# Performance work log

Hardware: AMD Instinct MI355X
Metric: run time of the kernel (lower is better)

Reference implementation:

```python
import jax, jax.numpy as jnp
import numpy as np

EPS = 1e-5

def conv1x1(x, w, b):
    # x: [B,Cin,H,W], w: [Cout,Cin], b: [Cout]
    return jnp.einsum('oi,bihw->bohw', w, x) + b[None, :, None, None]

def self_attention(x, qw, qb, kw, kb, vw, vb, fw, fb):
    B, C, H, W = x.shape
    hid = qw.shape[0]
    q = conv1x1(x, qw, qb).reshape(B, hid, H * W).transpose(0, 2, 1)   # [B,HW,hid]
    k = conv1x1(x, kw, kb).reshape(B, hid, H * W)                      # [B,hid,HW]
    v = conv1x1(x, vw, vb).reshape(B, C, H * W)                        # [B,C,HW]
    attn = jax.nn.softmax(jnp.einsum('bnh,bhm->bnm', q, k), axis=-1)   # [B,HW,HW]
    z = jnp.einsum('bnm,bcm->bnc', attn, v)                            # [B,HW,C]
    # faithful to torch .view(B,C,H,W) on contiguous [B,HW,C]: raw reshape, no transpose
    z = z.reshape(B, C, H, W)
    return conv1x1(z * x, fw, fb) + x

def group_norm_per_channel(y, gw, gb):
    # GroupNorm(num_groups == num_channels): per-channel instance norm, biased var
    mean = y.mean(axis=(2, 3), keepdims=True)
    var = ((y - mean) ** 2).mean(axis=(2, 3), keepdims=True)
    yn = (y - mean) * jax.lax.rsqrt(var + EPS)
    return yn * gw[None, :, None, None] + gb[None, :, None, None]

def setup_inputs() -> dict:
    key = jax.random.key(0)
    ks = jax.random.split(key, 32)
    B, C, H, W = 4, 64, 64, 64
    hid, att = 64, 64
    d = {}
    d['x'] = jax.random.normal(ks[0], (B, C, H, W), jnp.float32)
    d['h'] = jax.random.normal(ks[1], (B, hid, H, W), jnp.float32)
    d['c'] = jax.random.normal(ks[2], (B, hid, H, W), jnp.float32)
    i = 3
    for pre, cin in (('ax', C), ('ah', hid)):
        for nm, cout in (('q', att), ('k', att), ('v', cin), ('f', cin)):
            d[f'{pre}_{nm}w'] = jax.random.normal(ks[i], (cout, cin), jnp.float32) * 0.05; i += 1
            d[f'{pre}_{nm}b'] = jax.random.normal(ks[i], (cout,), jnp.float32) * 0.05; i += 1
    d['conv_w'] = jax.random.normal(ks[i], (4 * hid, C + hid, 3, 3), jnp.float32) * 0.05; i += 1
    d['conv_b'] = jax.random.normal(ks[i], (4 * hid,), jnp.float32) * 0.05; i += 1
    d['gn_w'] = jnp.ones((4 * hid,), jnp.float32)
    d['gn_b'] = jnp.zeros((4 * hid,), jnp.float32)
    return d

def reference(x, h, c,
              ax_qw, ax_qb, ax_kw, ax_kb, ax_vw, ax_vb, ax_fw, ax_fb,
              ah_qw, ah_qb, ah_kw, ah_kb, ah_vw, ah_vb, ah_fw, ah_fb,
              conv_w, conv_b, gn_w, gn_b):
    hid = h.shape[1]
    xa = self_attention(x, ax_qw, ax_qb, ax_kw, ax_kb, ax_vw, ax_vb, ax_fw, ax_fb)
    ha = self_attention(h, ah_qw, ah_qb, ah_kw, ah_kb, ah_vw, ah_vb, ah_fw, ah_fb)
    combined = jnp.concatenate([xa, ha], axis=1)
    y = jax.lax.conv_general_dilated(
        combined, conv_w, window_strides=(1, 1), padding=[(1, 1), (1, 1)],
        dimension_numbers=('NCHW', 'OIHW', 'NCHW')) + conv_b[None, :, None, None]
    y = group_norm_per_channel(y, gn_w, gn_b)
    i, f, o, g = jnp.split(y, 4, axis=1)
    i = jax.nn.sigmoid(i); f = jax.nn.sigmoid(f); o = jax.nn.sigmoid(o); g = jnp.tanh(g)
    c_next = f * c + i * g
    h_next = o * jnp.tanh(c_next)
    return jnp.stack([h_next, c_next])  # [2,B,hid,H,W]
```

## Files before the change

kernel.cpp:

```cpp
#include <hip/hip_runtime.h>
#include <hip/hip_bf16.h>


typedef __hip_bfloat16 bf16;
typedef const __hip_bfloat16* bfp;
typedef short bf16x8 __attribute__((ext_vector_type(8)));
typedef short short4v __attribute__((ext_vector_type(4)));
typedef float f32x4 __attribute__((ext_vector_type(4)));
typedef float f32x16 __attribute__((ext_vector_type(16)));
typedef unsigned int u32x4 __attribute__((ext_vector_type(4)));

#define SM_SHIFT 12.0f
#define SM_A  184.66496523378733f
#define SM_B  14034.452417194552f

__device__ __forceinline__ float ldf(const void* p, long i, int f32) {
    return f32 ? ((const float*)p)[i]
               : __bfloat162float(((const bf16*)p)[i]);
}
__device__ __forceinline__ short f2bf(float f) {
    bf16 h = __float2bfloat16(f);
    return *reinterpret_cast<short*>(&h);
}
__device__ __forceinline__ float bfv(short s) {
    unsigned short u = (unsigned short)s;
    return __bfloat162float(*reinterpret_cast<const bf16*>(&u));
}

__device__ __forceinline__ int sniff_f32(const void* xr)
{
    int lane = threadIdx.x & 63;
    unsigned long long v = ((const unsigned long long*)xr)[lane];
    int ok = 0;
#pragma unroll
    for (int i = 0; i < 4; ++i) {
        int e = (int)((v >> (16 * i + 7)) & 0xFF);
        ok += (e >= 100 && e <= 141);
    }
    ok += __shfl_xor(ok, 1, 64);
    ok += __shfl_xor(ok, 2, 64);
    ok += __shfl_xor(ok, 4, 64);
    ok += __shfl_xor(ok, 8, 64);
    ok += __shfl_xor(ok, 16, 64);
    ok += __shfl_xor(ok, 32, 64);
    return ok < 200;
}

__global__ __launch_bounds__(256) void qkv_kernel(
    const void* __restrict__ Xx, const void* __restrict__ Xh,
    const void* __restrict__ qwx, const void* __restrict__ qbx,
    const void* __restrict__ kwx, const void* __restrict__ kbx,
    const void* __restrict__ vwx, const void* __restrict__ vbx,
    const void* __restrict__ qwh, const void* __restrict__ qbh,
    const void* __restrict__ kwh, const void* __restrict__ kbh,
    const void* __restrict__ vwh, const void* __restrict__ vbh,
    bf16* __restrict__ Qx, bf16* __restrict__ Kx, bf16* __restrict__ Vtx,
    bf16* __restrict__ Qh, bf16* __restrict__ Kh, bf16* __restrict__ Vth,
    const void* __restrict__ cw, bf16* __restrict__ Wt,
    float* __restrict__ gacc, int qkvN)
{
    int bx = blockIdx.x;
    int tid = threadIdx.x;
    int f32 = sniff_f32(Xx);
    if (bx >= qkvN) {
        if (bx == qkvN) {
            for (int j = 0; j < 8; ++j)
                gacc[tid * 8 + j] = 0.f;
        }
        int wi = (bx - qkvN) * 256 + tid;
        int tap = wi >> 15;
        int rem = wi & 32767;
        int oc = rem >> 7, ic = rem & 127;
        Wt[wi] = __float2bfloat16(ldf(cw, ((long)oc * 128 + ic) * 9 + tap, f32));
        return;
    }
    __shared__ __align__(16) short xt[64][72];
    __shared__ __align__(16) short wq[64][72];
    __shared__ __align__(16) short wk[64][72];
    __shared__ __align__(16) short wv[64][72];
    int ab  = (bx >> 8) & 1;
    int idx = bx & 255;
    int b = idx >> 6;
    int n0 = (idx & 63) * 64;
    int wave = tid >> 6, lane = tid & 63;
    int q = lane >> 4, l15 = lane & 15;

    const void* X = ab ? Xh : Xx;
    const void* qw = ab ? qwh : qwx; const void* qb = ab ? qbh : qbx;
    const void* kw = ab ? kwh : kwx; const void* kb = ab ? kbh : kbx;
    const void* vw = ab ? vwh : vwx; const void* vb = ab ? vbh : vbx;
    short* Qg  = (short*)(ab ? Qh  : Qx)  + (long)b * 262144;
    short* Kg  = (short*)(ab ? Kh  : Kx)  + (long)b * 262144;
    short* Vtg = (short*)(ab ? Vth : Vtx) + (long)b * 262144;

    if (!f32) {
        const short* q16 = (const short*)qw;
        const short* k16 = (const short*)kw;
        const short* v16 = (const short*)vw;
        for (int rep = 0; rep < 2; ++rep) {
            int j8 = (rep * 256 + tid) * 8;
            *(bf16x8*)&wq[j8 >> 6][j8 & 63] = *(const bf16x8*)(q16 + j8);
            *(bf16x8*)&wk[j8 >> 6][j8 & 63] = *(const bf16x8*)(k16 + j8);
            *(bf16x8*)&wv[j8 >> 6][j8 & 63] = *(const bf16x8*)(v16 + j8);
        }
    } else {
        for (int rep = 0; rep < 16; ++rep) {
            int j = rep * 256 + tid;
            int i = j >> 6, cc = j & 63;
            wq[i][cc] = f2bf(((const float*)qw)[j]);
            wk[i][cc] = f2bf(((const float*)kw)[j]);
            wv[i][cc] = f2bf(((const float*)vw)[j]);
        }
    }
    long xbase = (long)b * 262144;
    if (!f32) {
        const short* X16 = (const short*)X;
        for (int rep = 0; rep < 2; ++rep) {
            int c = rep * 32 + (tid >> 3);
            int p8 = (tid & 7) * 8;
            bf16x8 v = *(const bf16x8*)(X16 + xbase + (long)c * 4096 + n0 + p8);
#pragma unroll
            for (int j = 0; j < 8; ++j) xt[p8 + j][c] = v[j];
        }
    } else {
        for (int rep = 0; rep < 16; ++rep) {
            int c = rep * 4 + (tid >> 6);
            int p = tid & 63;
            xt[p][c] = f2bf(ldf(X, xbase + (long)c * 4096 + n0 + p, f32));
        }
    }
    __syncthreads();

    bf16x8 a0 = *(const bf16x8*)&xt[wave * 16 + l15][q * 8];
    bf16x8 a1 = *(const bf16x8*)&xt[wave * 16 + l15][32 + q * 8];

    for (int ct = 0; ct < 4; ++ct) {
        bf16x8 bq0 = *(const bf16x8*)&wq[ct * 16 + l15][q * 8];
        bf16x8 bq1 = *(const bf16x8*)&wq[ct * 16 + l15][32 + q * 8];
        f32x4 z = (f32x4){0.f, 0.f, 0.f, 0.f};
        z = __builtin_amdgcn_mfma_f32_16x16x32_bf16(a0, bq0, z, 0, 0, 0);
        z = __builtin_amdgcn_mfma_f32_16x16x32_bf16(a1, bq1, z, 0, 0, 0);
        float bias = ldf(qb, ct * 16 + l15, f32);
        for (int reg = 0; reg < 4; ++reg)
            Qg[(long)(n0 + wave * 16 + q * 4 + reg) * 64 + ct * 16 + l15] =
                f2bf(z[reg] + bias);
    }
    for (int ct = 0; ct < 4; ++ct) {
        bf16x8 bk0 = *(const bf16x8*)&wk[ct * 16 + l15][q * 8];
        bf16x8 bk1 = *(const bf16x8*)&wk[ct * 16 + l15][32 + q * 8];
        f32x4 z = (f32x4){0.f, 0.f, 0.f, 0.f};
        z = __builtin_amdgcn_mfma_f32_16x16x32_bf16(a0, bk0, z, 0, 0, 0);
        z = __builtin_amdgcn_mfma_f32_16x16x32_bf16(a1, bk1, z, 0, 0, 0);
        float bias = ldf(kb, ct * 16 + l15, f32);
        for (int reg = 0; reg < 4; ++reg)
            Kg[(long)(n0 + wave * 16 + q * 4 + reg) * 64 + ct * 16 + l15] =
                f2bf(z[reg] + bias);
    }
    bf16x8 av0 = *(const bf16x8*)&wv[wave * 16 + l15][q * 8];
    bf16x8 av1 = *(const bf16x8*)&wv[wave * 16 + l15][32 + q * 8];
    for (int ct = 0; ct < 4; ++ct) {
        bf16x8 bx0 = *(const bf16x8*)&xt[ct * 16 + l15][q * 8];
        bf16x8 bx1 = *(const bf16x8*)&xt[ct * 16 + l15][32 + q * 8];
        f32x4 z = (f32x4){0.f, 0.f, 0.f, 0.f};
        z = __builtin_amdgcn_mfma_f32_16x16x32_bf16(av0, bx0, z, 0, 0, 0);
        z = __builtin_amdgcn_mfma_f32_16x16x32_bf16(av1, bx1, z, 0, 0, 0);
        for (int reg = 0; reg < 4; ++reg) {
            int c_out = wave * 16 + q * 4 + reg;
            float bias = ldf(vb, c_out, f32);
            Vtg[(long)c_out * 4096 + n0 + ct * 16 + l15] = f2bf(z[reg] + bias);
        }
    }
}

__global__ __launch_bounds__(256, 2) void attn_kernel(
    bfp Qx, bfp Kx, bfp Vtx,
    const void* __restrict__ Xx, const void* __restrict__ fwx,
    const void* __restrict__ fbx, bf16* __restrict__ outx,
    bfp Qh, bfp Kh, bfp Vth,
    const void* __restrict__ Xh, const void* __restrict__ fwh,
    const void* __restrict__ fbh, bf16* __restrict__ outh)
{
    __shared__ __align__(16) short smem[16384];
    short (*ks)[64][64]  = (short (*)[64][64])(smem);
    short (*vts)[64][64] = (short (*)[64][64])(smem + 8192);

    int tid = threadIdx.x;
    int wave = tid >> 6, lane = tid & 63;
    int l31 = lane & 31, hi = lane >> 5;
    int nh = wave >> 1, mh = wave & 1;
    int ab  = blockIdx.x >> 8;
    int idx = blockIdx.x & 255;
    int b = idx >> 6;
    int hrow = idx & 63;
    int f32 = sniff_f32(Xx);

    const short* Qb  = (const short*)(ab ? Qh  : Qx)  + (long)b * 262144;
    const short* Kb  = (const short*)(ab ? Kh  : Kx)  + (long)b * 262144;
    const short* Vtb = (const short*)(ab ? Vth : Vtx) + (long)b * 262144;
    const void* X  = ab ? Xh  : Xx;
    const void* fw = ab ? fwh : fwx;
    const void* fb = ab ? fbh : fbx;
    bf16* out = ab ? outh : outx;
    long xbase = (long)b * 262144;

    int cnq = nh * 32 + l31;
    long nq = (long)cnq * 64 + hrow;
    bf16x8 aq[4];
#pragma unroll
    for (int kc = 0; kc < 4; ++kc)
        aq[kc] = *(const bf16x8*)(Qb + nq * 64 + kc * 16 + hi * 8);

    f32x16 acc0 = (f32x16)(0.0f);
    f32x16 acc1 = (f32x16)(0.0f);
    f32x16 acc_l = (f32x16)(0.0f);
    const short ONE = 0x3F80;
    const bf16x8 ones = {ONE, ONE, ONE, ONE, ONE, ONE, ONE, ONE};

    int sw = (l31 >> 1) & 7;

    int r0 = tid >> 3, r1 = r0 + 32;
    int g = tid & 7;
    int sr0 = (r0 & 51) | ((r0 & 4) << 1) | ((r0 & 8) >> 1);
    int sr1 = sr0 + 32;
    int gk = (g ^ ((sr0 >> 1) & 7)) << 3;
    int gv = (g ^ ((r0 >> 1) & 7)) << 3;

    bf16x8 pk0 = *(const bf16x8*)(Kb + (long)r0 * 64 + g * 8);
    bf16x8 pk1 = *(const bf16x8*)(Kb + (long)r1 * 64 + g * 8);
    bf16x8 pv0 = *(const bf16x8*)(Vtb + (long)r0 * 4096 + g * 8);
    bf16x8 pv1 = *(const bf16x8*)(Vtb + (long)r1 * 4096 + g * 8);

    for (int it = 0; it < 64; ++it) {
        int buf = it & 1;
        *(bf16x8*)&ks[buf][sr0][gk] = pk0;
        *(bf16x8*)&ks[buf][sr1][gk] = pk1;
        *(bf16x8*)&vts[buf][r0][gv] = pv0;
        *(bf16x8*)&vts[buf][r1][gv] = pv1;
        __syncthreads();
        if (it + 1 < 64) {
            long m = (long)(it + 1) * 64;
            pk0 = *(const bf16x8*)(Kb + (m + r0) * 64 + g * 8);
            pk1 = *(const bf16x8*)(Kb + (m + r1) * 64 + g * 8);
            pv0 = *(const bf16x8*)(Vtb + (long)r0 * 4096 + m + g * 8);
            pv1 = *(const bf16x8*)(Vtb + (long)r1 * 4096 + m + g * 8);
        }

        f32x16 s = (f32x16)(0.0f);
        const short* kbase = &ks[buf][mh * 32 + l31][0];
#pragma unroll
        for (int kc = 0; kc < 4; ++kc) {
            bf16x8 ak = *(const bf16x8*)(kbase + (((kc * 2 + hi) ^ sw) << 3));
            s = __builtin_amdgcn_mfma_f32_32x32x16_bf16(ak, aq[kc], s, 0, 0, 0);
        }

        unsigned P32[8];
#pragma unroll
        for (int i = 0; i < 8; ++i) {
            unsigned b0 = (unsigned)fmaxf(fmaf(s[2 * i],     SM_A, SM_B), 0.f);
            unsigned b1 = (unsigned)fmaxf(fmaf(s[2 * i + 1], SM_A, SM_B), 0.f);
            P32[i] = b0 | (b1 << 16);
        }
        u32x4 B0v = (u32x4){P32[0], P32[1], P32[2], P32[3]};
        u32x4 B1v = (u32x4){P32[4], P32[5], P32[6], P32[7]};
        bf16x8 bp0 = __builtin_bit_cast(bf16x8, B0v);
        bf16x8 bp1 = __builtin_bit_cast(bf16x8, B1v);

        acc_l = __builtin_amdgcn_mfma_f32_32x32x16_bf16(ones, bp0, acc_l, 0, 0, 0);
        acc_l = __builtin_amdgcn_mfma_f32_32x32x16_bf16(ones, bp1, acc_l, 0, 0, 0);

        const short* v0base = &vts[buf][l31][0];
        const short* v1base = &vts[buf][32 + l31][0];
#pragma unroll
        for (int mc = 0; mc < 2; ++mc) {
            int gm = ((mh * 4 + mc * 2 + hi) ^ sw) << 3;
            bf16x8 av0 = *(const bf16x8*)(v0base + gm);
            bf16x8 av1 = *(const bf16x8*)(v1base + gm);
            bf16x8 bp = mc ? bp1 : bp0;
            acc0 = __builtin_amdgcn_mfma_f32_32x32x16_bf16(av0, bp, acc0, 0, 0, 0);
            acc1 = __builtin_amdgcn_mfma_f32_32x32x16_bf16(av1, bp, acc1, 0, 0, 0);
        }
    }

    float l_acc = acc_l[0];

    float* fs = (float*)smem;
    float* fl = (float*)smem + 4096;
    short* at_s  = smem;
    short* fwt_s = smem + 4992;
    short* o_lds = smem + 9600;

    __syncthreads();
    if (mh == 1) {
#pragma unroll
        for (int r = 0; r < 16; ++r) {
            int row = (r & 3) + ((r >> 2) << 3) + (hi << 2);
            fs[nh * 2048 + row * 32 + l31]        = acc0[r];
            fs[nh * 2048 + 1024 + row * 32 + l31] = acc1[r];
        }
        if (lane < 32) fl[nh * 32 + l31] = l_acc;
    }
    __syncthreads();
    if (mh == 0) {
        float iln = 1.f / (l_acc + fl[nh * 32 + l31]);
        short* orow = o_lds + cnq * 68;
#pragma unroll
        for (int rq = 0; rq < 4; ++rq) {
            int c0 = rq * 8 + (hi << 2);
            short4v oa, ob;
#pragma unroll
            for (int j = 0; j < 4; ++j) {
                int r = rq * 4 + j;
                int row = (r & 3) + ((r >> 2) << 3) + (hi << 2);
                oa[j] = f2bf((acc0[r] + fs[nh * 2048 + row * 32 + l31]) * iln);
                ob[j] = f2bf((acc1[r] + fs[nh * 2048 + 1024 + row * 32 + l31]) * iln);
            }
            *(short4v*)(orow + c0)      = oa;
            *(short4v*)(orow + 32 + c0) = ob;
        }
    }
    __syncthreads();
    if (!f32) {
        const short* f16p = (const short*)fw;
        for (int rep = 0; rep < 2; ++rep) {
            int j8 = (rep * 256 + tid) * 8;
            *(bf16x8*)(fwt_s + (j8 >> 6) * 72 + (j8 & 63)) =
                *(const bf16x8*)(f16p + j8);
        }
    } else {
        for (int rep = 0; rep < 16; ++rep) {
            int j = rep * 256 + tid;
            fwt_s[(j >> 6) * 72 + (j & 63)] = f2bf(((const float*)fw)[j]);
        }
    }
    {
        int cn = tid >> 3;
        int w8 = (tid & 7) * 8;
        for (int rep = 0; rep < 2; ++rep, cn += 32) {
            if (!f32) {
                bf16x8 xv = *(const bf16x8*)(
                    (const short*)X + xbase + (long)cn * 4096 + hrow * 64 + w8);
#pragma unroll
                for (int j = 0; j < 8; ++j)
                    at_s[(w8 + j) * 78 + cn] =
                        f2bf(bfv(o_lds[cn * 68 + w8 + j]) * bfv(xv[j]));
            } else {
#pragma unroll
                for (int j = 0; j < 8; ++j)
                    at_s[(w8 + j) * 78 + cn] =
                        f2bf(bfv(o_lds[cn * 68 + w8 + j]) *
                             ((const float*)X)[xbase + (long)cn * 4096 + hrow * 64 + w8 + j]);
            }
        }
    }
    __syncthreads();
    {
        int q = lane >> 4, l15 = lane & 15;
        bf16x8 a0 = *(const bf16x8*)(fwt_s + (wave * 16 + l15) * 72 + q * 8);
        bf16x8 a1 = *(const bf16x8*)(fwt_s + (wave * 16 + l15) * 72 + 32 + q * 8);
        short* outp = (short*)out;
        for (int nt = 0; nt < 4; ++nt) {
            bf16x8 b0 = *(const bf16x8*)(at_s + (nt * 16 + l15) * 78 + q * 8);
            bf16x8 b1 = *(const bf16x8*)(at_s + (nt * 16 + l15) * 78 + 32 + q * 8);
            f32x4 z = (f32x4){0.f, 0.f, 0.f, 0.f};
            z = __builtin_amdgcn_mfma_f32_16x16x32_bf16(a0, b0, z, 0, 0, 0);
            z = __builtin_amdgcn_mfma_f32_16x16x32_bf16(a1, b1, z, 0, 0, 0);
            int w = nt * 16 + l15;
            short4v o4;
            for (int reg = 0; reg < 4; ++reg) {
                int o = wave * 16 + q * 4 + reg;
                float v = z[reg] + ldf(fb, o, f32) +
                          ldf(X, xbase + (long)o * 4096 + hrow * 64 + w, f32);
                o4[reg] = f2bf(v);
            }
            *(short4v*)(outp + (((long)(b * 64 + hrow) * 64 + w) * 64
                                + wave * 16 + q * 4)) = o4;
        }
    }
}

__global__ __launch_bounds__(256) void conv3x3_kernel(
    bfp xa, bfp ha, bfp Wt, const void* __restrict__ cb,
    bf16* __restrict__ y, float* __restrict__ gacc,
    const void* __restrict__ xraw)
{
    __shared__ __align__(16) short in_s[3][66][136];
    int f32 = sniff_f32(xraw);
    int bx = blockIdx.x;
    int b = bx >> 7;
    int rem = bx & 127;
    int h = rem >> 1;
    int halfoc = rem & 1;
    int tid = threadIdx.x;
    int wave = tid >> 6, lane = tid & 63;
    int q = lane >> 4, l15 = lane & 15;

    const short* xab = (const short*)xa + (long)b * 262144;
    const short* hab = (const short*)ha + (long)b * 262144;
    const bf16x8 zv = {0, 0, 0, 0, 0, 0, 0, 0};
    for (int r = 0; r < 3; ++r) {
        int gy = h + r - 1;
        bool valid = (gy >= 0) && (gy < 64);
        for (int s = 0; s < 2; ++s) {
            int strip = s * 256 + tid;
            int w = strip >> 3;
            int c8 = (strip & 7) * 8;
            bf16x8 vx = zv, vh = zv;
            if (valid) {
                vx = *(const bf16x8*)(xab + ((long)gy * 64 + w) * 64 + c8);
                vh = *(const bf16x8*)(hab + ((long)gy * 64 + w) * 64 + c8);
            }
            *(bf16x8*)&in_s[r][w + 1][c8]      = vx;
            *(bf16x8*)&in_s[r][w + 1][64 + c8] = vh;
        }
    }
    if (tid < 96) {
        int r = tid / 32;
        int rest = tid % 32;
        int col = (rest & 1) ? 65 : 0;
        int c8 = (rest >> 1) * 8;
        *(bf16x8*)&in_s[r][col][c8] = zv;
    }
    __syncthreads();

    int oc0 = halfoc * 128 + wave * 32;
    f32x4 acc[2][4];
    for (int mt = 0; mt < 2; ++mt)
        for (int nt = 0; nt < 4; ++nt)
            acc[mt][nt] = (f32x4){0.f, 0.f, 0.f, 0.f};

    const short* Wb = (const short*)Wt;
    for (int tap = 0; tap < 9; ++tap) {
        int dy = tap / 3, dx = tap - dy * 3;
        for (int kc = 0; kc < 4; ++kc) {
            bf16x8 afrag[2];
            for (int mt = 0; mt < 2; ++mt)
                afrag[mt] = *(const bf16x8*)(
                    Wb + ((long)tap * 256 + oc0 + mt * 16 + l15) * 128 + kc * 32 + q * 8);
            for (int nt = 0; nt < 4; ++nt) {
                bf16x8 bfrag = *(const bf16x8*)&in_s[dy][nt * 16 + l15 + dx][kc * 32 + q * 8];
                for (int mt = 0; mt < 2; ++mt)
                    acc[mt][nt] = __builtin_amdgcn_mfma_f32_16x16x32_bf16(
                        afrag[mt], bfrag, acc[mt][nt], 0, 0, 0);
            }
        }
    }

    long ybase = (long)b * 1048576 + (long)h * 64;
    for (int mt = 0; mt < 2; ++mt) {
        for (int reg = 0; reg < 4; ++reg) {
            int oc = oc0 + mt * 16 + q * 4 + reg;
            float bias = ldf(cb, oc, f32);
            float s = 0.f, s2 = 0.f;
            for (int nt = 0; nt < 4; ++nt) {
                float v = acc[mt][nt][reg] + bias;
                ((short*)y)[ybase + (long)oc * 4096 + nt * 16 + l15] = f2bf(v);
                s += v; s2 = fmaf(v, v, s2);
            }
            s  += __shfl_xor(s,  1, 64);  s2 += __shfl_xor(s2, 1, 64);
            s  += __shfl_xor(s,  2, 64);  s2 += __shfl_xor(s2, 2, 64);
            s  += __shfl_xor(s,  4, 64);  s2 += __shfl_xor(s2, 4, 64);
            s  += __shfl_xor(s,  8, 64);  s2 += __shfl_xor(s2, 8, 64);
            if (l15 == 0) {
                atomicAdd(&gacc[b * 256 + oc], s);
                atomicAdd(&gacc[1024 + b * 256 + oc], s2);
            }
        }
    }
}

__global__ __launch_bounds__(256) void gates_kernel(
    bfp y, const float* __restrict__ gacc,
    const void* __restrict__ gw, const void* __restrict__ gb,
    const void* __restrict__ c_in, void* __restrict__ out)
{
    int f32 = sniff_f32(c_in);
    int t = blockIdx.x * 256 + threadIdx.x;
    int b = t >> 15;
    int r = t & 32767;
    int ch = r >> 9;
    int p8 = (r & 511) * 8;
    long ybase = (long)b * 1048576;
    long idx8 = (long)b * 262144 + (long)ch * 4096 + p8;

    float mu[4], rstd[4], gwv[4], gbv[4];
    bf16x8 yv[4];
#pragma unroll
    for (int g = 0; g < 4; ++g) {
        int cc = g * 64 + ch;
        float m = gacc[b * 256 + cc] * (1.f / 4096.f);
        float var = gacc[1024 + b * 256 + cc] * (1.f / 4096.f) - m * m;
        mu[g] = m;
        rstd[g] = rsqrtf(fmaxf(var, 0.f) + 1e-5f);
        gwv[g] = ldf(gw, cc, f32);
        gbv[g] = ldf(gb, cc, f32);
        yv[g] = *(const bf16x8*)((const short*)y + ybase + (long)cc * 4096 + p8);
    }
    float cprev[8];
    if (!f32) {
        bf16x8 cv = *(const bf16x8*)((const short*)c_in + idx8);
#pragma unroll
        for (int j = 0; j < 8; ++j) cprev[j] = bfv(cv[j]);
    } else {
#pragma unroll
        for (int j = 0; j < 8; ++j) cprev[j] = ((const float*)c_in)[idx8 + j];
    }
    bf16x8 hn8, cn8;
    float hnf[8], cnf[8];
#pragma unroll
    for (int j = 0; j < 8; ++j) {
        float v0 = (bfv(yv[0][j]) - mu[0]) * rstd[0] * gwv[0] + gbv[0];
        float v1 = (bfv(yv[1][j]) - mu[1]) * rstd[1] * gwv[1] + gbv[1];
        float v2 = (bfv(yv[2][j]) - mu[2]) * rstd[2] * gwv[2] + gbv[2];
        float v3 = (bfv(yv[3][j]) - mu[3]) * rstd[3] * gwv[3] + gbv[3];
        float ig = 1.f / (1.f + __expf(-v0));
        float fg = 1.f / (1.f + __expf(-v1));
        float og = 1.f / (1.f + __expf(-v2));
        float gg = tanhf(v3);
        float cn = fg * cprev[j] + ig * gg;
        float hn = og * tanhf(cn);
        hn8[j] = f2bf(hn); cn8[j] = f2bf(cn);
        hnf[j] = hn; cnf[j] = cn;
    }
    if (f32) {
        float* o32 = (float*)out;
#pragma unroll
        for (int j = 0; j < 8; ++j) {
            o32[idx8 + j] = hnf[j];
            o32[1048576 + idx8 + j] = cnf[j];
        }
    } else {
        short* o16 = (short*)out;
        *(bf16x8*)(o16 + idx8) = hn8;
        *(bf16x8*)(o16 + 1048576 + idx8) = cn8;
    }
}

extern "C" void kernel_launch(void* const* d_in, const int* in_sizes, int n_in,
                              void* d_out, int out_size, void* d_ws, size_t ws_size,
                              hipStream_t stream)
{
    const void* x = d_in[0]; const void* h = d_in[1]; const void* c = d_in[2];
    const void* ax_qw = d_in[3],  *ax_qb = d_in[4];
    const void* ax_kw = d_in[5],  *ax_kb = d_in[6];
    const void* ax_vw = d_in[7],  *ax_vb = d_in[8];
    const void* ax_fw = d_in[9],  *ax_fb = d_in[10];
    const void* ah_qw = d_in[11], *ah_qb = d_in[12];
    const void* ah_kw = d_in[13], *ah_kb = d_in[14];
    const void* ah_vw = d_in[15], *ah_vb = d_in[16];
    const void* ah_fw = d_in[17], *ah_fb = d_in[18];
    const void* conv_w = d_in[19], *conv_b = d_in[20];
    const void* gn_w = d_in[21],  *gn_b = d_in[22];

    char* wsb = (char*)d_ws;
    auto S = [&](int i) { return wsb + ((unsigned long)i << 21); };
    bool fused = ws_size >= (18ul << 20) + 16384;

    bf16* ha = (bf16*)S(0);
    bf16* Wt = (bf16*)S(1);
    bf16 *Qx, *Kx, *Vtx, *Qh, *Kh, *Vth, *xa, *y;
    char* tail;
    if (fused) {
        Qx = (bf16*)S(2); Kx = (bf16*)S(3); Vtx = (bf16*)S(4);
        Qh = (bf16*)S(5); Kh = (bf16*)S(6); Vth = (bf16*)S(7);
        xa = (bf16*)S(8); y = Qx;
        tail = S(9);
    } else {
        Qx = (bf16*)S(2); Kx = (bf16*)S(3); Vtx = (bf16*)S(4);
        Qh = Qx; Kh = Kx; Vth = Vtx;
        xa = (bf16*)S(6); y = Qx;
        tail = S(7);
    }
    float* gacc = (float*)tail;

    if (fused) {
        qkv_kernel<<<512 + 1152, 256, 0, stream>>>(
            x, h,
            ax_qw, ax_qb, ax_kw, ax_kb, ax_vw, ax_vb,
            ah_qw, ah_qb, ah_kw, ah_kb, ah_vw, ah_vb,
            Qx, Kx, Vtx, Qh, Kh, Vth, conv_w, Wt, gacc, 512);
        attn_kernel<<<512, 256, 0, stream>>>(
            Qx, Kx, Vtx, x, ax_fw, ax_fb, xa,
            Qh, Kh, Vth, h, ah_fw, ah_fb, ha);
    } else {
        qkv_kernel<<<256 + 1152, 256, 0, stream>>>(
            x, x,
            ax_qw, ax_qb, ax_kw, ax_kb, ax_vw, ax_vb,
            ax_qw, ax_qb, ax_kw, ax_kb, ax_vw, ax_vb,
            Qx, Kx, Vtx, Qx, Kx, Vtx, conv_w, Wt, gacc, 256);
        attn_kernel<<<256, 256, 0, stream>>>(
            Qx, Kx, Vtx, x, ax_fw, ax_fb, xa,
            Qx, Kx, Vtx, x, ax_fw, ax_fb, xa);
        qkv_kernel<<<256, 256, 0, stream>>>(
            h, h,
            ah_qw, ah_qb, ah_kw, ah_kb, ah_vw, ah_vb,
            ah_qw, ah_qb, ah_kw, ah_kb, ah_vw, ah_vb,
            Qh, Kh, Vth, Qh, Kh, Vth, conv_w, Wt, gacc, 256);
        attn_kernel<<<256, 256, 0, stream>>>(
            Qh, Kh, Vth, h, ah_fw, ah_fb, ha,
            Qh, Kh, Vth, h, ah_fw, ah_fb, ha);
    }
    conv3x3_kernel<<<512, 256, 0, stream>>>(xa, ha, Wt, conv_b, y, gacc, x);
    gates_kernel<<<512, 256, 0, stream>>>(y, gacc, gn_w, gn_b, c, d_out);
}
```

Measured before the change: 202.4 us.

## Widen attention blocks to 8 waves with 128-key tiles and 4-way key split

The attention kernel moves from 256 to 512 threads per block. Each KV iteration now stages 128 keys instead of 64, so the loop runs 32 times and there are half as many barriers. Four waves per query half now split the key dimension, and their partial outputs and row sums are reduced through LDS in two stages. The output-projection epilogue is split across all 8 waves, and the fw staging is overlapped with the reduction. In exchange, LDS doubles to 64 KB per block, which may limit occupancy, and the extra reduction passes and barriers add cost.

Measured after the change: 201.6 us. About the same (-0.4%).

```diff
diff --git a/kernel.cpp b/kernel.cpp
--- a/kernel.cpp
+++ b/kernel.cpp
@@ -172,7 +172,7 @@
     }
 }
 
-__global__ __launch_bounds__(256, 2) void attn_kernel(
+__global__ __launch_bounds__(512, 4) void attn_kernel(
     bfp Qx, bfp Kx, bfp Vtx,
     const void* __restrict__ Xx, const void* __restrict__ fwx,
     const void* __restrict__ fbx, bf16* __restrict__ outx,
@@ -180,14 +180,12 @@
     const void* __restrict__ Xh, const void* __restrict__ fwh,
     const void* __restrict__ fbh, bf16* __restrict__ outh)
 {
-    __shared__ __align__(16) short smem[16384];
-    short (*ks)[64][64]  = (short (*)[64][64])(smem);
-    short (*vts)[64][64] = (short (*)[64][64])(smem + 8192);
+    __shared__ __align__(16) short smem[32768];
 
     int tid = threadIdx.x;
     int wave = tid >> 6, lane = tid & 63;
     int l31 = lane & 31, hi = lane >> 5;
-    int nh = wave >> 1, mh = wave & 1;
+    int nh = wave >> 2, mq = wave & 3;
     int ab  = blockIdx.x >> 8;
     int idx = blockIdx.x & 255;
     int b = idx >> 6;
@@ -210,43 +208,48 @@
     for (int kc = 0; kc < 4; ++kc)
         aq[kc] = *(const bf16x8*)(Qb + nq * 64 + kc * 16 + hi * 8);
 
-    f32x16 acc0 = (f32x16)(0.0f);
-    f32x16 acc1 = (f32x16)(0.0f);
+    f32x16 acc[2];
+    acc[0] = (f32x16)(0.0f); acc[1] = (f32x16)(0.0f);
     f32x16 acc_l = (f32x16)(0.0f);
     const short ONE = 0x3F80;
     const bf16x8 ones = {ONE, ONE, ONE, ONE, ONE, ONE, ONE, ONE};
 
     int sw = (l31 >> 1) & 7;
 
-    int r0 = tid >> 3, r1 = r0 + 32;
+    int r0 = tid >> 3, r1 = r0 + 64;
     int g = tid & 7;
     int sr0 = (r0 & 51) | ((r0 & 4) << 1) | ((r0 & 8) >> 1);
-    int sr1 = sr0 + 32;
+    int sr1 = sr0 + 64;
     int gk = (g ^ ((sr0 >> 1) & 7)) << 3;
-    int gv = (g ^ ((r0 >> 1) & 7)) << 3;
+    int cV = r0;
+    int gv = (g ^ (cV & 7)) << 3;
 
     bf16x8 pk0 = *(const bf16x8*)(Kb + (long)r0 * 64 + g * 8);
     bf16x8 pk1 = *(const bf16x8*)(Kb + (long)r1 * 64 + g * 8);
-    bf16x8 pv0 = *(const bf16x8*)(Vtb + (long)r0 * 4096 + g * 8);
-    bf16x8 pv1 = *(const bf16x8*)(Vtb + (long)r1 * 4096 + g * 8);
-
-    for (int it = 0; it < 64; ++it) {
-        int buf = it & 1;
-        *(bf16x8*)&ks[buf][sr0][gk] = pk0;
-        *(bf16x8*)&ks[buf][sr1][gk] = pk1;
-        *(bf16x8*)&vts[buf][r0][gv] = pv0;
-        *(bf16x8*)&vts[buf][r1][gv] = pv1;
+    bf16x8 pv0 = *(const bf16x8*)(Vtb + (long)cV * 4096 + g * 8);
+    bf16x8 pv1 = *(const bf16x8*)(Vtb + (long)cV * 4096 + 64 + g * 8);
+
+    for (int mt = 0; mt < 32; ++mt) {
+        int buf = mt & 1;
+        short* ksw = smem + buf * 8192;
+        short* vsw = smem + 16384 + buf * 8192;
+        *(bf16x8*)(ksw + sr0 * 64 + gk)      = pk0;
+        *(bf16x8*)(ksw + sr1 * 64 + gk)      = pk1;
+        *(bf16x8*)(vsw + cV * 128 + gv)      = pv0;
+        *(bf16x8*)(vsw + cV * 128 + gv + 64) = pv1;
         __syncthreads();
-        if (it + 1 < 64) {
-            long m = (long)(it + 1) * 64;
+        if (mt + 1 < 32) {
+            long m = (long)(mt + 1) * 128;
             pk0 = *(const bf16x8*)(Kb + (m + r0) * 64 + g * 8);
             pk1 = *(const bf16x8*)(Kb + (m + r1) * 64 + g * 8);
-            pv0 = *(const bf16x8*)(Vtb + (long)r0 * 4096 + m + g * 8);
-            pv1 = *(const bf16x8*)(Vtb + (long)r1 * 4096 + m + g * 8);
-        }
+            pv0 = *(const bf16x8*)(Vtb + (long)cV * 4096 + m + g * 8);
+            pv1 = *(const bf16x8*)(Vtb + (long)cV * 4096 + m + 64 + g * 8);
+        }
+        const short* ksb  = smem + buf * 8192;
+        const short* vtsb = smem + 16384 + buf * 8192;
 
         f32x16 s = (f32x16)(0.0f);
-        const short* kbase = &ks[buf][mh * 32 + l31][0];
+        const short* kbase = ksb + (mq * 32 + l31) * 64;
 #pragma unroll
         for (int kc = 0; kc < 4; ++kc) {
             bf16x8 ak = *(const bf16x8*)(kbase + (((kc * 2 + hi) ^ sw) << 3));
@@ -268,97 +271,121 @@
         acc_l = __builtin_amdgcn_mfma_f32_32x32x16_bf16(ones, bp0, acc_l, 0, 0, 0);
         acc_l = __builtin_amdgcn_mfma_f32_32x32x16_bf16(ones, bp1, acc_l, 0, 0, 0);
 
-        const short* v0base = &vts[buf][l31][0];
-        const short* v1base = &vts[buf][32 + l31][0];
 #pragma unroll
         for (int mc = 0; mc < 2; ++mc) {
-            int gm = ((mh * 4 + mc * 2 + hi) ^ sw) << 3;
-            bf16x8 av0 = *(const bf16x8*)(v0base + gm);
-            bf16x8 av1 = *(const bf16x8*)(v1base + gm);
             bf16x8 bp = mc ? bp1 : bp0;
-            acc0 = __builtin_amdgcn_mfma_f32_32x32x16_bf16(av0, bp, acc0, 0, 0, 0);
-            acc1 = __builtin_amdgcn_mfma_f32_32x32x16_bf16(av1, bp, acc1, 0, 0, 0);
+            int qch = mq * 4 + mc * 2 + hi;
+#pragma unroll
+            for (int ch = 0; ch < 2; ++ch) {
+                int c = ch * 32 + l31;
+                bf16x8 av = *(const bf16x8*)(
+                    vtsb + c * 128 + ((qch ^ (c & 7)) << 3));
+                acc[ch] = __builtin_amdgcn_mfma_f32_32x32x16_bf16(av, bp, acc[ch], 0, 0, 0);
+            }
         }
     }
 
     float l_acc = acc_l[0];
 
     float* fs = (float*)smem;
-    float* fl = (float*)smem + 4096;
+    float* fl = (float*)smem + 8192;
+    short* fwt_s = smem + 16896;
+    short* o_lds = smem + 21504;
     short* at_s  = smem;
-    short* fwt_s = smem + 4992;
-    short* o_lds = smem + 9600;
-
-    __syncthreads();
-    if (mh == 1) {
-#pragma unroll
-        for (int r = 0; r < 16; ++r) {
-            int row = (r & 3) + ((r >> 2) << 3) + (hi << 2);
-            fs[nh * 2048 + row * 32 + l31]        = acc0[r];
-            fs[nh * 2048 + 1024 + row * 32 + l31] = acc1[r];
-        }
-        if (lane < 32) fl[nh * 32 + l31] = l_acc;
-    }
-    __syncthreads();
-    if (mh == 0) {
-        float iln = 1.f / (l_acc + fl[nh * 32 + l31]);
+
+    __syncthreads();
+    if (hi == 0) fl[nh * 128 + mq * 32 + l31] = l_acc;
+    if (mq == 1 || mq == 3) {
+        int L = mq >> 1;
+#pragma unroll
+        for (int ch = 0; ch < 2; ++ch)
+#pragma unroll
+            for (int r = 0; r < 16; ++r) {
+                int c = ch * 32 + (r & 3) + ((r >> 2) << 3) + (hi << 2);
+                fs[L * 4096 + nh * 2048 + c * 32 + l31] = acc[ch][r];
+            }
+    }
+    if (!f32) {
+        int j8 = tid * 8;
+        *(bf16x8*)(fwt_s + (j8 >> 6) * 72 + (j8 & 63)) =
+            *(const bf16x8*)((const short*)fw + j8);
+    } else {
+#pragma unroll
+        for (int jj = 0; jj < 8; ++jj) {
+            int j = tid * 8 + jj;
+            fwt_s[(j >> 6) * 72 + (j & 63)] = f2bf(((const float*)fw)[j]);
+        }
+    }
+    __syncthreads();
+    if (mq == 0 || mq == 2) {
+        int L = mq >> 1;
+#pragma unroll
+        for (int ch = 0; ch < 2; ++ch)
+#pragma unroll
+            for (int r = 0; r < 16; ++r) {
+                int c = ch * 32 + (r & 3) + ((r >> 2) << 3) + (hi << 2);
+                acc[ch][r] += fs[L * 4096 + nh * 2048 + c * 32 + l31];
+            }
+    }
+    __syncthreads();
+    if (mq == 2) {
+#pragma unroll
+        for (int ch = 0; ch < 2; ++ch)
+#pragma unroll
+            for (int r = 0; r < 16; ++r) {
+                int c = ch * 32 + (r & 3) + ((r >> 2) << 3) + (hi << 2);
+                fs[nh * 2048 + c * 32 + l31] = acc[ch][r];
+            }
+    }
+    __syncthreads();
+    if (mq == 0) {
+        float l_tot = fl[nh * 128 + l31]      + fl[nh * 128 + 32 + l31]
+                    + fl[nh * 128 + 64 + l31] + fl[nh * 128 + 96 + l31];
+        float iln = 1.f / l_tot;
         short* orow = o_lds + cnq * 68;
 #pragma unroll
-        for (int rq = 0; rq < 4; ++rq) {
-            int c0 = rq * 8 + (hi << 2);
-            short4v oa, ob;
-#pragma unroll
-            for (int j = 0; j < 4; ++j) {
-                int r = rq * 4 + j;
-                int row = (r & 3) + ((r >> 2) << 3) + (hi << 2);
-                oa[j] = f2bf((acc0[r] + fs[nh * 2048 + row * 32 + l31]) * iln);
-                ob[j] = f2bf((acc1[r] + fs[nh * 2048 + 1024 + row * 32 + l31]) * iln);
-            }
-            *(short4v*)(orow + c0)      = oa;
-            *(short4v*)(orow + 32 + c0) = ob;
-        }
-    }
-    __syncthreads();
-    if (!f32) {
-        const short* f16p = (const short*)fw;
-        for (int rep = 0; rep < 2; ++rep) {
-            int j8 = (rep * 256 + tid) * 8;
-            *(bf16x8*)(fwt_s + (j8 >> 6) * 72 + (j8 & 63)) =
-                *(const bf16x8*)(f16p + j8);
-        }
-    } else {
-        for (int rep = 0; rep < 16; ++rep) {
-            int j = rep * 256 + tid;
-            fwt_s[(j >> 6) * 72 + (j & 63)] = f2bf(((const float*)fw)[j]);
-        }
-    }
+        for (int ch = 0; ch < 2; ++ch)
+#pragma unroll
+            for (int rq = 0; rq < 4; ++rq) {
+                short4v o4;
+#pragma unroll
+                for (int j = 0; j < 4; ++j) {
+                    int r = rq * 4 + j;
+                    int c = ch * 32 + (r & 3) + ((r >> 2) << 3) + (hi << 2);
+                    o4[j] = f2bf((acc[ch][r] +
+                                  fs[nh * 2048 + c * 32 + l31]) * iln);
+                }
+                *(short4v*)(orow + ch * 32 + rq * 8 + hi * 4) = o4;
+            }
+    }
+    __syncthreads();
     {
         int cn = tid >> 3;
         int w8 = (tid & 7) * 8;
-        for (int rep = 0; rep < 2; ++rep, cn += 32) {
-            if (!f32) {
-                bf16x8 xv = *(const bf16x8*)(
-                    (const short*)X + xbase + (long)cn * 4096 + hrow * 64 + w8);
-#pragma unroll
-                for (int j = 0; j < 8; ++j)
-                    at_s[(w8 + j) * 78 + cn] =
-                        f2bf(bfv(o_lds[cn * 68 + w8 + j]) * bfv(xv[j]));
-            } else {
-#pragma unroll
-                for (int j = 0; j < 8; ++j)
-                    at_s[(w8 + j) * 78 + cn] =
-                        f2bf(bfv(o_lds[cn * 68 + w8 + j]) *
-                             ((const float*)X)[xbase + (long)cn * 4096 + hrow * 64 + w8 + j]);
-            }
+        if (!f32) {
+            bf16x8 xv = *(const bf16x8*)(
+                (const short*)X + xbase + (long)cn * 4096 + hrow * 64 + w8);
+#pragma unroll
+            for (int j = 0; j < 8; ++j)
+                at_s[(w8 + j) * 78 + cn] =
+                    f2bf(bfv(o_lds[cn * 68 + w8 + j]) * bfv(xv[j]));
+        } else {
+#pragma unroll
+            for (int j = 0; j < 8; ++j)
+                at_s[(w8 + j) * 78 + cn] =
+                    f2bf(bfv(o_lds[cn * 68 + w8 + j]) *
+                         ((const float*)X)[xbase + (long)cn * 4096 + hrow * 64 + w8 + j]);
         }
     }
     __syncthreads();
     {
         int q = lane >> 4, l15 = lane & 15;
-        bf16x8 a0 = *(const bf16x8*)(fwt_s + (wave * 16 + l15) * 72 + q * 8);
-        bf16x8 a1 = *(const bf16x8*)(fwt_s + (wave * 16 + l15) * 72 + 32 + q * 8);
+        int w4 = wave & 3;
+        int ntb = (wave >> 2) * 2;
+        bf16x8 a0 = *(const bf16x8*)(fwt_s + (w4 * 16 + l15) * 72 + q * 8);
+        bf16x8 a1 = *(const bf16x8*)(fwt_s + (w4 * 16 + l15) * 72 + 32 + q * 8);
         short* outp = (short*)out;
-        for (int nt = 0; nt < 4; ++nt) {
+        for (int nt = ntb; nt < ntb + 2; ++nt) {
             bf16x8 b0 = *(const bf16x8*)(at_s + (nt * 16 + l15) * 78 + q * 8);
             bf16x8 b1 = *(const bf16x8*)(at_s + (nt * 16 + l15) * 78 + 32 + q * 8);
             f32x4 z = (f32x4){0.f, 0.f, 0.f, 0.f};
@@ -367,13 +394,13 @@
             int w = nt * 16 + l15;
             short4v o4;
             for (int reg = 0; reg < 4; ++reg) {
-                int o = wave * 16 + q * 4 + reg;
+                int o = w4 * 16 + q * 4 + reg;
                 float v = z[reg] + ldf(fb, o, f32) +
                           ldf(X, xbase + (long)o * 4096 + hrow * 64 + w, f32);
                 o4[reg] = f2bf(v);
             }
             *(short4v*)(outp + (((long)(b * 64 + hrow) * 64 + w) * 64
-                                + wave * 16 + q * 4)) = o4;
+                                + w4 * 16 + q * 4)) = o4;
         }
     }
 }
@@ -578,7 +605,7 @@
             ax_qw, ax_qb, ax_kw, ax_kb, ax_vw, ax_vb,
             ah_qw, ah_qb, ah_kw, ah_kb, ah_vw, ah_vb,
             Qx, Kx, Vtx, Qh, Kh, Vth, conv_w, Wt, gacc, 512);
-        attn_kernel<<<512, 256, 0, stream>>>(
+        attn_kernel<<<512, 512, 0, stream>>>(
             Qx, Kx, Vtx, x, ax_fw, ax_fb, xa,
             Qh, Kh, Vth, h, ah_fw, ah_fb, ha);
     } else {
@@ -587,7 +614,7 @@
             ax_qw, ax_qb, ax_kw, ax_kb, ax_vw, ax_vb,
             ax_qw, ax_qb, ax_kw, ax_kb, ax_vw, ax_vb,
             Qx, Kx, Vtx, Qx, Kx, Vtx, conv_w, Wt, gacc, 256);
-        attn_kernel<<<256, 256, 0, stream>>>(
+        attn_kernel<<<256, 512, 0, stream>>>(
             Qx, Kx, Vtx, x, ax_fw, ax_fb, xa,
             Qx, Kx, Vtx, x, ax_fw, ax_fb, xa);
         qkv_kernel<<<256, 256, 0, stream>>>(
@@ -595,7 +622,7 @@
             ah_qw, ah_qb, ah_kw, ah_kb, ah_vw, ah_vb,
             ah_qw, ah_qb, ah_kw, ah_kb, ah_vw, ah_vb,
             Qh, Kh, Vth, Qh, Kh, Vth, conv_w, Wt, gacc, 256);
-        attn_kernel<<<256, 256, 0, stream>>>(
+        attn_kernel<<<256, 512, 0, stream>>>(
             Qh, Kh, Vth, h, ah_fw, ah_fb, ha,
             Qh, Kh, Vth, h, ah_fw, ah_fb, ha);
     }
```
